# Optimization experiments

Hardware: AMD Instinct MI355X
Metric: run time of the kernel (lower is better)

Reference implementation:

```python
import jax, jax.numpy as jnp
import numpy as np

N_NODE = 50000
N_EDGE = 600000
BATCH = 64
IN_DIM = 128
OUT_DIM = 128
ATTN_DIM = 128
N_REL_IDS = 2 * 237 + 1  # 475 relation embedding rows


def setup_inputs() -> dict:
    key = jax.random.key(0)
    ks = jax.random.split(key, 16)
    s = 1.0 / np.sqrt(IN_DIM)
    return {
        "q_sub": jax.random.randint(ks[0], (BATCH,), 0, N_NODE, dtype=jnp.int32),
        "q_rel": jax.random.randint(ks[1], (BATCH,), 0, N_REL_IDS, dtype=jnp.int32),
        "r_idx": jax.random.randint(ks[2], (N_EDGE,), 0, BATCH, dtype=jnp.int32),
        "hidden": jax.random.normal(ks[3], (N_NODE, IN_DIM), dtype=jnp.float32),
        "edge_sub": jax.random.randint(ks[4], (N_EDGE,), 0, N_NODE, dtype=jnp.int32),
        "edge_rel": jax.random.randint(ks[5], (N_EDGE,), 0, N_REL_IDS, dtype=jnp.int32),
        "edge_obj": jax.random.randint(ks[6], (N_EDGE,), 0, N_NODE, dtype=jnp.int32),
        "n_node": N_NODE,
        "rela_embed": jax.random.normal(ks[7], (N_REL_IDS, IN_DIM), dtype=jnp.float32),
        "Ws": jax.random.normal(ks[8], (IN_DIM, ATTN_DIM), dtype=jnp.float32) * s,
        "Wr": jax.random.normal(ks[9], (IN_DIM, ATTN_DIM), dtype=jnp.float32) * s,
        "Wqr_w": jax.random.normal(ks[10], (IN_DIM, ATTN_DIM), dtype=jnp.float32) * s,
        "Wqr_b": jax.random.normal(ks[11], (ATTN_DIM,), dtype=jnp.float32) * s,
        "wa_w": jax.random.normal(ks[12], (ATTN_DIM,), dtype=jnp.float32) * s,
        "wa_b": jax.random.normal(ks[13], (), dtype=jnp.float32) * s,
        "Wh": jax.random.normal(ks[14], (IN_DIM, OUT_DIM), dtype=jnp.float32) * s,
    }


def reference(q_sub, q_rel, r_idx, hidden, edge_sub, edge_rel, edge_obj, n_node,
              rela_embed, Ws, Wr, Wqr_w, Wqr_b, wa_w, wa_b, Wh):
    # gather: per-edge subject hidden state and relation embedding
    hs = hidden[edge_sub]            # [E, in_dim]
    hr = rela_embed[edge_rel]        # [E, in_dim]
    h_qr = rela_embed[q_rel][r_idx]  # [E, in_dim] query-relation embed per edge
    message = hs * hr                # [E, in_dim]
    # attention MLP: sigmoid(w_alpha(relu(Ws hs + Wr hr + Wqr h_qr + b)))
    pre = jax.nn.relu(hs @ Ws + hr @ Wr + h_qr @ Wqr_w + Wqr_b)  # [E, attn]
    alpha = jax.nn.sigmoid(pre @ wa_w + wa_b)                    # [E]
    message = alpha[:, None] * message
    # scatter-add into object node buckets
    message_agg = jax.ops.segment_sum(message, edge_obj, num_segments=n_node)  # [n_node, in_dim]
    # final linear, act = identity (default)
    return message_agg @ Wh
```

## Files before the change

### kernel.cpp

```cpp
#include <hip/hip_runtime.h>

typedef float f32x4 __attribute__((ext_vector_type(4)));
typedef _Float16 f16x8 __attribute__((ext_vector_type(8)));
typedef _Float16 v2h __attribute__((ext_vector_type(2)));
typedef short s16x2 __attribute__((ext_vector_type(2)));

#define NB 128

__device__ __forceinline__ float hdot2(v2h a, v2h b, float c) {
#if __has_builtin(__builtin_amdgcn_fdot2)
  return __builtin_amdgcn_fdot2(a, b, c, false);
#else
  return c + (float)a[0] * (float)b[0] + (float)a[1] * (float)b[1];
#endif
}

__device__ __forceinline__ v2h relu2(v2h a) {
#if __has_builtin(__builtin_elementwise_max)
  const v2h z = {(_Float16)0, (_Float16)0};
  return __builtin_elementwise_max(a, z);
#else
  const v2h z = {(_Float16)0, (_Float16)0};
  s16x2 m = a > z;
  s16x2 bits = *(s16x2*)&a;
  s16x2 r = bits & m;
  return *(v2h*)&r;
#endif
}

__global__ __launch_bounds__(256) void part_hist(const int* __restrict__ eobj,
                                                 int* __restrict__ ghist,
                                                 int E, int nbkt, int chunk) {
  __shared__ int lh[128];
  const int b = blockIdx.x, t = threadIdx.x;
  for (int i = t; i < nbkt; i += 256) lh[i] = 0;
  __syncthreads();
  const int lo = b * chunk, hi = min(lo + chunk, E);
  for (int i = lo + t; i < hi; i += 256) atomicAdd(&lh[eobj[i] >> 9], 1);
  __syncthreads();
  for (int i = t; i < nbkt; i += 256) ghist[i * NB + b] = lh[i];
}

__global__ __launch_bounds__(256) void part_scatter(
    const int* __restrict__ eobj, const int* __restrict__ esub,
    const int* __restrict__ erel, const int* __restrict__ ridx,
    const int* __restrict__ qrel, const int* __restrict__ ghist,
    int* __restrict__ bstart, int* __restrict__ offs,
    int2* __restrict__ tmp, int E, int n, int nbkt, int chunk) {
  __shared__ int s[128];
  __shared__ int scur[128];
  const int b = blockIdx.x, t = threadIdx.x;

  int pre = 0, tot = 0;
  if (t < nbkt) {
#pragma unroll 8
    for (int k = 0; k < NB; ++k) {
      const int v = ghist[t * NB + k];
      pre += (k < b) ? v : 0;
      tot += v;
    }
  }
  if (t < 128) s[t] = (t < nbkt) ? tot : 0;
  __syncthreads();
  if (t < 128) {
    for (int o = 1; o < 128; o <<= 1) {
      const int a = (t >= o) ? s[t - o] : 0;
      __syncthreads();
      s[t] += a;
      __syncthreads();
    }
  } else {
    for (int o = 1; o < 128; o <<= 1) { __syncthreads(); __syncthreads(); }
  }
  if (t < nbkt) {
    const int bucket_start = s[t] - tot;
    scur[t] = bucket_start + pre;
    if (b == 0) bstart[t] = bucket_start;
  }
  if (b == 0 && t == 0) { bstart[nbkt] = E; offs[n] = E; }
  __syncthreads();

  const int lo = b * chunk, hi = min(lo + chunk, E);
  for (int i = lo + t; i < hi; i += 256) {
    const int obj = eobj[i];
    const int bkt = obj >> 9;
    const int p = atomicAdd(&scur[bkt], 1);
    tmp[p] = make_int2(esub[i], (erel[i] << 18) | (qrel[ridx[i]] << 9) | (obj & 511));
  }
}

__global__ __launch_bounds__(256) void bucket_sort(
    const int2* __restrict__ tmp, const int* __restrict__ bstart,
    int* __restrict__ offs, int2* __restrict__ ssrq, int n) {
  __shared__ int2 stage[8192];
  __shared__ int scnt[512];
  __shared__ int scur[512];
  const int b = blockIdx.x, t = threadIdx.x;
  const int s0 = bstart[b], s1 = bstart[b + 1];
  const int cnt = s1 - s0;
  const int node0 = b * 512;

  scnt[t] = 0;
  scnt[t + 256] = 0;
  __syncthreads();
  for (int i = t; i < cnt; i += 256) atomicAdd(&scnt[tmp[s0 + i].y & 511], 1);
  __syncthreads();

  const int d0 = scnt[t], d1 = scnt[t + 256];
  __syncthreads();
  for (int o = 1; o < 512; o <<= 1) {
    const int a0 = (t >= o) ? scnt[t - o] : 0;
    const int a1 = (t + 256 >= o) ? scnt[t + 256 - o] : 0;
    __syncthreads();
    scnt[t] += a0;
    scnt[t + 256] += a1;
    __syncthreads();
  }
  const int e0 = scnt[t] - d0, e1 = scnt[t + 256] - d1;
  scur[t] = e0;
  scur[t + 256] = e1;
  if (node0 + t < n) offs[node0 + t] = s0 + e0;
  if (node0 + t + 256 < n) offs[node0 + t + 256] = s0 + e1;
  __syncthreads();

  if (cnt <= 8192) {
    for (int i = t; i < cnt; i += 256) {
      const int2 p = tmp[s0 + i];
      const int q = atomicAdd(&scur[p.y & 511], 1);
      stage[q] = make_int2(p.x, p.y >> 9);
    }
    __syncthreads();
    for (int i = t; i < cnt; i += 256) ssrq[s0 + i] = stage[i];
  } else {
    for (int i = t; i < cnt; i += 256) {
      const int2 p = tmp[s0 + i];
      const int q = atomicAdd(&scur[p.y & 511], 1);
      ssrq[s0 + q] = make_int2(p.x, p.y >> 9);
    }
  }
}

__global__ __launch_bounds__(256) void prep_gemm(
    const float* __restrict__ hidden, const float* __restrict__ rela,
    const float* __restrict__ Ws, const float* __restrict__ Wr,
    const float* __restrict__ Wqr, const float* __restrict__ Wqr_b,
    _Float16* __restrict__ Hcat, _Float16* __restrict__ Rcat,
    _Float16* __restrict__ Rwqrt, int n_node, int n_rel,
    int hid_blocks, int rel_blocks) {
  __shared__ _Float16 sW[16384];
  const int bidx = blockIdx.x;
  const float* A;
  const float* W;
  const float* bias = nullptr;
  _Float16* Lo = nullptr;
  _Float16* Chi;
  int M, bb, ldc, coff;
  if (bidx < hid_blocks) {
    bb = bidx; A = hidden; W = Ws; Lo = Hcat; Chi = Hcat;
    M = n_node; ldc = 256; coff = 128;
  } else if (bidx < hid_blocks + rel_blocks) {
    bb = bidx - hid_blocks; A = rela; W = Wr; Lo = Rcat; Chi = Rcat;
    M = n_rel; ldc = 256; coff = 128;
  } else {
    bb = bidx - hid_blocks - rel_blocks; A = rela; W = Wqr; Chi = Rwqrt;
    bias = Wqr_b; M = n_rel; ldc = 128; coff = 0;
  }

  for (int i = threadIdx.x; i < 16384; i += 256) {
    const int k = i >> 7, c = i & 127;
    sW[(k >> 3) * 1024 + c * 8 + (k & 7)] = (_Float16)W[i];
  }
  __syncthreads();

  const int wv = threadIdx.x >> 6, l = threadIdx.x & 63;
  const int row = bb * 64 + wv * 16 + (l & 15);
  const int kb = (l >> 4) * 8;
  const bool rvalid = row < M;

  f16x8 a[4];
#pragma unroll
  for (int kk = 0; kk < 4; ++kk) {
    f16x8 t = {0, 0, 0, 0, 0, 0, 0, 0};
    if (rvalid) {
      const f32x4 lo = *(const f32x4*)(A + (size_t)row * 128 + kb + 32 * kk);
      const f32x4 hi = *(const f32x4*)(A + (size_t)row * 128 + kb + 32 * kk + 4);
      t[0] = (_Float16)lo[0]; t[1] = (_Float16)lo[1];
      t[2] = (_Float16)lo[2]; t[3] = (_Float16)lo[3];
      t[4] = (_Float16)hi[0]; t[5] = (_Float16)hi[1];
      t[6] = (_Float16)hi[2]; t[7] = (_Float16)hi[3];
      if (Lo) *(f16x8*)(Lo + (size_t)row * 256 + kb + 32 * kk) = t;
    }
    a[kk] = t;
  }

  f32x4 acc[8];
#pragma unroll
  for (int n = 0; n < 8; ++n) acc[n] = (f32x4){0.f, 0.f, 0.f, 0.f};
#pragma unroll
  for (int n = 0; n < 8; ++n)
#pragma unroll
    for (int kk = 0; kk < 4; ++kk) {
      const int kg = 4 * kk + (l >> 4);
      const f16x8 bfrag = *(const f16x8*)(sW + kg * 1024 + (16 * n + (l & 15)) * 8);
      acc[n] = __builtin_amdgcn_mfma_f32_16x16x32_f16(a[kk], bfrag, acc[n], 0, 0, 0);
    }

  const int orow_base = bb * 64 + wv * 16 + (l >> 4) * 4;
#pragma unroll
  for (int n = 0; n < 8; ++n) {
    const int col = 16 * n + (l & 15);
    const float badd = bias ? bias[col] : 0.0f;
#pragma unroll
    for (int r4 = 0; r4 < 4; ++r4) {
      const int orow = orow_base + r4;
      if (orow < M)
        Chi[(size_t)orow * ldc + coff + col] = (_Float16)(acc[n][r4] + badd);
    }
  }
}

__global__ __launch_bounds__(256) void gemm_final(
    const _Float16* __restrict__ agg, const float* __restrict__ Wh,
    float* __restrict__ out, int M) {
  __shared__ _Float16 sW[16384];
  for (int i = threadIdx.x; i < 16384; i += 256) {
    const int k = i >> 7, c = i & 127;
    sW[(k >> 3) * 1024 + c * 8 + (k & 7)] = (_Float16)Wh[i];
  }
  __syncthreads();

  const int wv = threadIdx.x >> 6, l = threadIdx.x & 63;
  const int row = blockIdx.x * 64 + wv * 16 + (l & 15);
  const int kb = (l >> 4) * 8;
  const bool rvalid = row < M;

  f16x8 a[4];
#pragma unroll
  for (int kk = 0; kk < 4; ++kk) {
    f16x8 t = {0, 0, 0, 0, 0, 0, 0, 0};
    if (rvalid) t = *(const f16x8*)(agg + (size_t)row * 128 + kb + 32 * kk);
    a[kk] = t;
  }

  f32x4 acc[8];
#pragma unroll
  for (int n = 0; n < 8; ++n) acc[n] = (f32x4){0.f, 0.f, 0.f, 0.f};
#pragma unroll
  for (int n = 0; n < 8; ++n)
#pragma unroll
    for (int kk = 0; kk < 4; ++kk) {
      const int kg = 4 * kk + (l >> 4);
      const f16x8 bfrag = *(const f16x8*)(sW + kg * 1024 + (16 * n + (l & 15)) * 8);
      acc[n] = __builtin_amdgcn_mfma_f32_16x16x32_f16(a[kk], bfrag, acc[n], 0, 0, 0);
    }

  const int orow_base = blockIdx.x * 64 + wv * 16 + (l >> 4) * 4;
#pragma unroll
  for (int n = 0; n < 8; ++n) {
    const int col = 16 * n + (l & 15);
#pragma unroll
    for (int r4 = 0; r4 < 4; ++r4) {
      const int orow = orow_base + r4;
      if (orow < M) out[(size_t)orow * 128 + col] = acc[n][r4];
    }
  }
}

__global__ __launch_bounds__(256) void reduce_f16(
    const int2* __restrict__ ssrq, const int* __restrict__ offs,
    const _Float16* __restrict__ Hcat, const _Float16* __restrict__ Rcat,
    const _Float16* __restrict__ Rwqrt, const float* __restrict__ wa_w,
    const float* __restrict__ wa_b_p, _Float16* __restrict__ agg, int n_node) {
  const int node = (blockIdx.x * blockDim.x + threadIdx.x) >> 6;
  if (node >= n_node) return;
  const int l = threadIdx.x & 63;
  const int g = l >> 4;
  const int d0 = (l & 15) * 8;

  v2h wa2[4];
  {
    const float4 w0 = *(const float4*)(wa_w + d0);
    const float4 w1 = *(const float4*)(wa_w + d0 + 4);
    wa2[0] = (v2h){(_Float16)w0.x, (_Float16)w0.y};
    wa2[1] = (v2h){(_Float16)w0.z, (_Float16)w0.w};
    wa2[2] = (v2h){(_Float16)w1.x, (_Float16)w1.y};
    wa2[3] = (v2h){(_Float16)w1.z, (_Float16)w1.w};
  }
  const float wab = wa_b_p[0];

  const int start = offs[node], end = offs[node + 1];
  v2h acc2[4] = {};

  for (int base = start; base < end; base += 64) {
    const int cnt = min(end - base, 64);
    int s_all = 0, rq_all = 0;
    if (l < cnt) { const int2 sr = ssrq[base + l]; s_all = sr.x; rq_all = sr.y; }
    for (int c = 0; c < cnt; c += 4) {
      const int src = c + g;
      const bool valid = src < cnt;
      const int sv = __shfl(s_all, src);
      const int rqv = __shfl(rq_all, src);
      const int rv = rqv >> 9, qv = rqv & 511;

      f32x4 rw = *(const f32x4*)(Hcat + ((size_t)sv << 8) + 128 + d0);
      f32x4 rr = *(const f32x4*)(Rcat + ((size_t)rv << 8) + 128 + d0);
      f32x4 rq = *(const f32x4*)(Rwqrt + ((size_t)qv << 7) + d0);
      f32x4 rh = *(const f32x4*)(Hcat + ((size_t)sv << 8) + d0);
      f32x4 rg = *(const f32x4*)(Rcat + ((size_t)rv << 8) + d0);
      const v2h* hw = (const v2h*)&rw;
      const v2h* hr_ = (const v2h*)&rr;
      const v2h* hq = (const v2h*)&rq;
      const v2h* hh = (const v2h*)&rh;
      const v2h* hg = (const v2h*)&rg;

      float part = 0.0f;
      v2h prod[4];
#pragma unroll
      for (int i = 0; i < 4; ++i) {
        const v2h pre = relu2(hw[i] + hr_[i] + hq[i]);
        part = hdot2(pre, wa2[i], part);
        prod[i] = hh[i] * hg[i];
      }
      part += __shfl_xor(part, 1);
      part += __shfl_xor(part, 2);
      part += __shfl_xor(part, 4);
      part += __shfl_xor(part, 8);
      const float alpha = valid ? 1.0f / (1.0f + __expf(-(part + wab))) : 0.0f;
      const _Float16 ah = (_Float16)alpha;
      const v2h alpha2 = {ah, ah};
#pragma unroll
      for (int i = 0; i < 4; ++i) acc2[i] += alpha2 * prod[i];
    }
  }

#pragma unroll
  for (int i = 0; i < 4; ++i) {
    unsigned x = *(unsigned*)&acc2[i];
    unsigned y = (unsigned)__shfl_xor((int)x, 16);
    acc2[i] += *(v2h*)&y;
    x = *(unsigned*)&acc2[i];
    y = (unsigned)__shfl_xor((int)x, 32);
    acc2[i] += *(v2h*)&y;
  }
  if (l < 16)
    *(f32x4*)(agg + (size_t)node * 128 + d0) = *(f32x4*)acc2;
}

extern "C" void kernel_launch(void* const* d_in, const int* in_sizes, int n_in,
                              void* d_out, int out_size, void* d_ws, size_t ws_size,
                              hipStream_t stream) {
  const int* q_rel = (const int*)d_in[1];
  const int* r_idx = (const int*)d_in[2];
  const float* hidden = (const float*)d_in[3];
  const int* edge_sub = (const int*)d_in[4];
  const int* edge_rel = (const int*)d_in[5];
  const int* edge_obj = (const int*)d_in[6];
  const float* rela = (const float*)d_in[8];
  const float* Ws = (const float*)d_in[9];
  const float* Wr = (const float*)d_in[10];
  const float* Wqr_w = (const float*)d_in[11];
  const float* Wqr_b = (const float*)d_in[12];
  const float* wa_w = (const float*)d_in[13];
  const float* wa_b = (const float*)d_in[14];
  const float* Wh = (const float*)d_in[15];

  const int E = in_sizes[2];
  const int n_node = in_sizes[3] / 128;
  const int n_rel = in_sizes[8] / 128;
  float* out = (float*)d_out;

  const int nbkt = (n_node + 511) / 512;
  const int chunk = (E + NB - 1) / NB;

  auto al = [](size_t x) { return (x + 511) & ~(size_t)511; };
  char* ws = (char*)d_ws;
  size_t o = 0;
  _Float16* Hcat = (_Float16*)(ws + o);  o += al((size_t)n_node * 256 * 2);
  _Float16* agg  = (_Float16*)(ws + o);  o += al((size_t)n_node * 128 * 2);
  _Float16* Rcat = (_Float16*)(ws + o);  o += al((size_t)n_rel * 256 * 2);
  _Float16* Rwqrt = (_Float16*)(ws + o); o += al((size_t)n_rel * 128 * 2);
  int* offs = (int*)(ws + o);      o += al((size_t)(n_node + 1) * 4);
  int* ghist = (int*)(ws + o);     o += al((size_t)nbkt * NB * 4);
  int* bstart = (int*)(ws + o);    o += al((size_t)(nbkt + 1) * 4);
  int2* tmp = (int2*)(ws + o);     o += al((size_t)E * 8);
  int2* ssrq = (int2*)(ws + o);    o += al((size_t)E * 8);

  part_hist<<<dim3(NB), dim3(256), 0, stream>>>(edge_obj, ghist, E, nbkt, chunk);
  part_scatter<<<dim3(NB), dim3(256), 0, stream>>>(
      edge_obj, edge_sub, edge_rel, r_idx, q_rel, ghist, bstart, offs,
      tmp, E, n_node, nbkt, chunk);
  bucket_sort<<<dim3(nbkt), dim3(256), 0, stream>>>(tmp, bstart, offs, ssrq, n_node);

  const int hid_blocks = (n_node + 63) / 64;
  const int rel_blocks = (n_rel + 63) / 64;
  prep_gemm<<<dim3(hid_blocks + 2 * rel_blocks), dim3(256), 0, stream>>>(
      hidden, rela, Ws, Wr, Wqr_w, Wqr_b, Hcat, Rcat, Rwqrt,
      n_node, n_rel, hid_blocks, rel_blocks);

  const int rblocks = (n_node * 64 + 255) / 256;
  reduce_f16<<<dim3(rblocks), dim3(256), 0, stream>>>(
      ssrq, offs, Hcat, Rcat, Rwqrt, wa_w, wa_b, agg, n_node);

  gemm_final<<<dim3(hid_blocks), dim3(256), 0, stream>>>(agg, Wh, out, n_node);
}
```

Before: 227.9 us.

## Compute edge attention in edge order and pack alpha with relation into sort keys

Per-edge attention is moved out of the segmented reduction into a new kernel that runs in original edge order. That kernel is fused with the partition histogram and writes an f16 alpha packed with the relation id per edge. The sort now carries the edge index, and bucket_sort looks up the packed alpha/relation word. The reduction then only gathers the H and R rows and does a multiply-accumulate. Hcat and Rcat are split into separate 128-wide arrays. This trades an extra pass over E edges and more gathers of the projected rows for a lighter, less irregular per-node reduction, at the cost of additional kernels and an extra global alpha array.

```diff
diff --git a/kernel.cpp b/kernel.cpp
--- a/kernel.cpp
+++ b/kernel.cpp
@@ -6,6 +6,8 @@
 typedef short s16x2 __attribute__((ext_vector_type(2)));
 
 #define NB 128
+
+union h16bits { _Float16 h; unsigned short u; };
 
 __device__ __forceinline__ float hdot2(v2h a, v2h b, float c) {
 #if __has_builtin(__builtin_amdgcn_fdot2)
@@ -28,124 +30,13 @@
 #endif
 }
 
-__global__ __launch_bounds__(256) void part_hist(const int* __restrict__ eobj,
-                                                 int* __restrict__ ghist,
-                                                 int E, int nbkt, int chunk) {
-  __shared__ int lh[128];
-  const int b = blockIdx.x, t = threadIdx.x;
-  for (int i = t; i < nbkt; i += 256) lh[i] = 0;
-  __syncthreads();
-  const int lo = b * chunk, hi = min(lo + chunk, E);
-  for (int i = lo + t; i < hi; i += 256) atomicAdd(&lh[eobj[i] >> 9], 1);
-  __syncthreads();
-  for (int i = t; i < nbkt; i += 256) ghist[i * NB + b] = lh[i];
-}
-
-__global__ __launch_bounds__(256) void part_scatter(
-    const int* __restrict__ eobj, const int* __restrict__ esub,
-    const int* __restrict__ erel, const int* __restrict__ ridx,
-    const int* __restrict__ qrel, const int* __restrict__ ghist,
-    int* __restrict__ bstart, int* __restrict__ offs,
-    int2* __restrict__ tmp, int E, int n, int nbkt, int chunk) {
-  __shared__ int s[128];
-  __shared__ int scur[128];
-  const int b = blockIdx.x, t = threadIdx.x;
-
-  int pre = 0, tot = 0;
-  if (t < nbkt) {
-#pragma unroll 8
-    for (int k = 0; k < NB; ++k) {
-      const int v = ghist[t * NB + k];
-      pre += (k < b) ? v : 0;
-      tot += v;
-    }
-  }
-  if (t < 128) s[t] = (t < nbkt) ? tot : 0;
-  __syncthreads();
-  if (t < 128) {
-    for (int o = 1; o < 128; o <<= 1) {
-      const int a = (t >= o) ? s[t - o] : 0;
-      __syncthreads();
-      s[t] += a;
-      __syncthreads();
-    }
-  } else {
-    for (int o = 1; o < 128; o <<= 1) { __syncthreads(); __syncthreads(); }
-  }
-  if (t < nbkt) {
-    const int bucket_start = s[t] - tot;
-    scur[t] = bucket_start + pre;
-    if (b == 0) bstart[t] = bucket_start;
-  }
-  if (b == 0 && t == 0) { bstart[nbkt] = E; offs[n] = E; }
-  __syncthreads();
-
-  const int lo = b * chunk, hi = min(lo + chunk, E);
-  for (int i = lo + t; i < hi; i += 256) {
-    const int obj = eobj[i];
-    const int bkt = obj >> 9;
-    const int p = atomicAdd(&scur[bkt], 1);
-    tmp[p] = make_int2(esub[i], (erel[i] << 18) | (qrel[ridx[i]] << 9) | (obj & 511));
-  }
-}
-
-__global__ __launch_bounds__(256) void bucket_sort(
-    const int2* __restrict__ tmp, const int* __restrict__ bstart,
-    int* __restrict__ offs, int2* __restrict__ ssrq, int n) {
-  __shared__ int2 stage[8192];
-  __shared__ int scnt[512];
-  __shared__ int scur[512];
-  const int b = blockIdx.x, t = threadIdx.x;
-  const int s0 = bstart[b], s1 = bstart[b + 1];
-  const int cnt = s1 - s0;
-  const int node0 = b * 512;
-
-  scnt[t] = 0;
-  scnt[t + 256] = 0;
-  __syncthreads();
-  for (int i = t; i < cnt; i += 256) atomicAdd(&scnt[tmp[s0 + i].y & 511], 1);
-  __syncthreads();
-
-  const int d0 = scnt[t], d1 = scnt[t + 256];
-  __syncthreads();
-  for (int o = 1; o < 512; o <<= 1) {
-    const int a0 = (t >= o) ? scnt[t - o] : 0;
-    const int a1 = (t + 256 >= o) ? scnt[t + 256 - o] : 0;
-    __syncthreads();
-    scnt[t] += a0;
-    scnt[t + 256] += a1;
-    __syncthreads();
-  }
-  const int e0 = scnt[t] - d0, e1 = scnt[t + 256] - d1;
-  scur[t] = e0;
-  scur[t + 256] = e1;
-  if (node0 + t < n) offs[node0 + t] = s0 + e0;
-  if (node0 + t + 256 < n) offs[node0 + t + 256] = s0 + e1;
-  __syncthreads();
-
-  if (cnt <= 8192) {
-    for (int i = t; i < cnt; i += 256) {
-      const int2 p = tmp[s0 + i];
-      const int q = atomicAdd(&scur[p.y & 511], 1);
-      stage[q] = make_int2(p.x, p.y >> 9);
-    }
-    __syncthreads();
-    for (int i = t; i < cnt; i += 256) ssrq[s0 + i] = stage[i];
-  } else {
-    for (int i = t; i < cnt; i += 256) {
-      const int2 p = tmp[s0 + i];
-      const int q = atomicAdd(&scur[p.y & 511], 1);
-      ssrq[s0 + q] = make_int2(p.x, p.y >> 9);
-    }
-  }
-}
-
 __global__ __launch_bounds__(256) void prep_gemm(
     const float* __restrict__ hidden, const float* __restrict__ rela,
     const float* __restrict__ Ws, const float* __restrict__ Wr,
     const float* __restrict__ Wqr, const float* __restrict__ Wqr_b,
-    _Float16* __restrict__ Hcat, _Float16* __restrict__ Rcat,
-    _Float16* __restrict__ Rwqrt, int n_node, int n_rel,
+    _Float16* __restrict__ Hlo, _Float16* __restrict__ Hws,
+    _Float16* __restrict__ Rlo, _Float16* __restrict__ Rwr,
+    _Float16* __restrict__ Rwqr, int n_node, int n_rel,
     int hid_blocks, int rel_blocks) {
   __shared__ _Float16 sW[16384];
   const int bidx = blockIdx.x;
@@ -153,17 +44,15 @@
   const float* W;
   const float* bias = nullptr;
   _Float16* Lo = nullptr;
-  _Float16* Chi;
-  int M, bb, ldc, coff;
+  _Float16* C;
+  int M, bb;
   if (bidx < hid_blocks) {
-    bb = bidx; A = hidden; W = Ws; Lo = Hcat; Chi = Hcat;
-    M = n_node; ldc = 256; coff = 128;
+    bb = bidx; A = hidden; W = Ws; Lo = Hlo; C = Hws; M = n_node;
   } else if (bidx < hid_blocks + rel_blocks) {
-    bb = bidx - hid_blocks; A = rela; W = Wr; Lo = Rcat; Chi = Rcat;
-    M = n_rel; ldc = 256; coff = 128;
+    bb = bidx - hid_blocks; A = rela; W = Wr; Lo = Rlo; C = Rwr; M = n_rel;
   } else {
-    bb = bidx - hid_blocks - rel_blocks; A = rela; W = Wqr; Chi = Rwqrt;
-    bias = Wqr_b; M = n_rel; ldc = 128; coff = 0;
+    bb = bidx - hid_blocks - rel_blocks; A = rela; W = Wqr; C = Rwqr;
+    bias = Wqr_b; M = n_rel;
   }
 
   for (int i = threadIdx.x; i < 16384; i += 256) {
@@ -188,7 +77,7 @@
       t[2] = (_Float16)lo[2]; t[3] = (_Float16)lo[3];
       t[4] = (_Float16)hi[0]; t[5] = (_Float16)hi[1];
       t[6] = (_Float16)hi[2]; t[7] = (_Float16)hi[3];
-      if (Lo) *(f16x8*)(Lo + (size_t)row * 256 + kb + 32 * kk) = t;
+      if (Lo) *(f16x8*)(Lo + (size_t)row * 128 + kb + 32 * kk) = t;
     }
     a[kk] = t;
   }
@@ -214,68 +103,37 @@
     for (int r4 = 0; r4 < 4; ++r4) {
       const int orow = orow_base + r4;
       if (orow < M)
-        Chi[(size_t)orow * ldc + coff + col] = (_Float16)(acc[n][r4] + badd);
-    }
-  }
-}
-
-__global__ __launch_bounds__(256) void gemm_final(
-    const _Float16* __restrict__ agg, const float* __restrict__ Wh,
-    float* __restrict__ out, int M) {
-  __shared__ _Float16 sW[16384];
-  for (int i = threadIdx.x; i < 16384; i += 256) {
-    const int k = i >> 7, c = i & 127;
-    sW[(k >> 3) * 1024 + c * 8 + (k & 7)] = (_Float16)Wh[i];
-  }
-  __syncthreads();
-
-  const int wv = threadIdx.x >> 6, l = threadIdx.x & 63;
-  const int row = blockIdx.x * 64 + wv * 16 + (l & 15);
-  const int kb = (l >> 4) * 8;
-  const bool rvalid = row < M;
-
-  f16x8 a[4];
-#pragma unroll
-  for (int kk = 0; kk < 4; ++kk) {
-    f16x8 t = {0, 0, 0, 0, 0, 0, 0, 0};
-    if (rvalid) t = *(const f16x8*)(agg + (size_t)row * 128 + kb + 32 * kk);
-    a[kk] = t;
-  }
-
-  f32x4 acc[8];
-#pragma unroll
-  for (int n = 0; n < 8; ++n) acc[n] = (f32x4){0.f, 0.f, 0.f, 0.f};
-#pragma unroll
-  for (int n = 0; n < 8; ++n)
-#pragma unroll
-    for (int kk = 0; kk < 4; ++kk) {
-      const int kg = 4 * kk + (l >> 4);
-      const f16x8 bfrag = *(const f16x8*)(sW + kg * 1024 + (16 * n + (l & 15)) * 8);
-      acc[n] = __builtin_amdgcn_mfma_f32_16x16x32_f16(a[kk], bfrag, acc[n], 0, 0, 0);
-    }
-
-  const int orow_base = blockIdx.x * 64 + wv * 16 + (l >> 4) * 4;
-#pragma unroll
-  for (int n = 0; n < 8; ++n) {
-    const int col = 16 * n + (l & 15);
-#pragma unroll
-    for (int r4 = 0; r4 < 4; ++r4) {
-      const int orow = orow_base + r4;
-      if (orow < M) out[(size_t)orow * 128 + col] = acc[n][r4];
-    }
-  }
-}
-
-__global__ __launch_bounds__(256) void reduce_f16(
-    const int2* __restrict__ ssrq, const int* __restrict__ offs,
-    const _Float16* __restrict__ Hcat, const _Float16* __restrict__ Rcat,
-    const _Float16* __restrict__ Rwqrt, const float* __restrict__ wa_w,
-    const float* __restrict__ wa_b_p, _Float16* __restrict__ agg, int n_node) {
-  const int node = (blockIdx.x * blockDim.x + threadIdx.x) >> 6;
-  if (node >= n_node) return;
-  const int l = threadIdx.x & 63;
+        C[(size_t)orow * 128 + col] = (_Float16)(acc[n][r4] + badd);
+    }
+  }
+}
+
+__global__ __launch_bounds__(256) void hist_alpha(
+    const int* __restrict__ eobj, const int* __restrict__ esub,
+    const int* __restrict__ erel, const int* __restrict__ ridx,
+    const int* __restrict__ qrel, const _Float16* __restrict__ Hws,
+    const _Float16* __restrict__ Rwr, const _Float16* __restrict__ Rwqr,
+    const float* __restrict__ wa_w, const float* __restrict__ wa_b_p,
+    int* __restrict__ ghist, int* __restrict__ ar,
+    int E, int nbkt, int chunk) {
+  __shared__ int lh[128];
+  const int bidx = blockIdx.x, t = threadIdx.x;
+
+  if (bidx < NB) {
+    for (int i = t; i < nbkt; i += 256) lh[i] = 0;
+    __syncthreads();
+    const int lo = bidx * chunk, hi = min(lo + chunk, E);
+    for (int i = lo + t; i < hi; i += 256) atomicAdd(&lh[eobj[i] >> 9], 1);
+    __syncthreads();
+    for (int i = t; i < nbkt; i += 256) ghist[i * NB + bidx] = lh[i];
+    return;
+  }
+
+  const int wv = t >> 6, l = t & 63;
   const int g = l >> 4;
   const int d0 = (l & 15) * 8;
+  const int aw = (bidx - NB) * 4 + wv;
+  const int nwaves = (gridDim.x - NB) * 4;
 
   v2h wa2[4];
   {
@@ -288,48 +146,182 @@
   }
   const float wab = wa_b_p[0];
 
+  for (int base = aw * 64; base < E; base += nwaves * 64) {
+    const int cnt = min(E - base, 64);
+    int s = 0, r = 0, q = 0;
+    if (l < cnt) {
+      const int i = base + l;
+      s = esub[i];
+      r = erel[i];
+      q = qrel[ridx[i]];
+    }
+    for (int c = 0; c < cnt; c += 4) {
+      const int src = c + g;
+      const bool valid = src < cnt;
+      const int sv = __shfl(s, src);
+      const int rv = __shfl(r, src);
+      const int qv = __shfl(q, src);
+
+      const f32x4 rw = *(const f32x4*)(Hws + ((size_t)sv << 7) + d0);
+      const f32x4 rr = *(const f32x4*)(Rwr + ((size_t)rv << 7) + d0);
+      const f32x4 rq = *(const f32x4*)(Rwqr + ((size_t)qv << 7) + d0);
+      const v2h* hw = (const v2h*)&rw;
+      const v2h* hr_ = (const v2h*)&rr;
+      const v2h* hq = (const v2h*)&rq;
+
+      float part = 0.0f;
+#pragma unroll
+      for (int i = 0; i < 4; ++i)
+        part = hdot2(relu2(hw[i] + hr_[i] + hq[i]), wa2[i], part);
+      part += __shfl_xor(part, 1);
+      part += __shfl_xor(part, 2);
+      part += __shfl_xor(part, 4);
+      part += __shfl_xor(part, 8);
+
+      if (valid && (l & 15) == 0) {
+        const float alpha = 1.0f / (1.0f + __expf(-(part + wab)));
+        h16bits hb;
+        hb.h = (_Float16)alpha;
+        ar[base + src] = (rv << 16) | hb.u;
+      }
+    }
+  }
+}
+
+__global__ __launch_bounds__(256) void part_scatter(
+    const int* __restrict__ eobj, const int* __restrict__ esub,
+    const int* __restrict__ ghist, int* __restrict__ bstart,
+    int* __restrict__ offs, int2* __restrict__ tmp,
+    int E, int n, int nbkt, int chunk) {
+  __shared__ int s[128];
+  __shared__ int scur[128];
+  const int b = blockIdx.x, t = threadIdx.x;
+
+  int pre = 0, tot = 0;
+  if (t < nbkt) {
+#pragma unroll 8
+    for (int k = 0; k < NB; ++k) {
+      const int v = ghist[t * NB + k];
+      pre += (k < b) ? v : 0;
+      tot += v;
+    }
+  }
+  if (t < 128) s[t] = (t < nbkt) ? tot : 0;
+  __syncthreads();
+  if (t < 128) {
+    for (int o = 1; o < 128; o <<= 1) {
+      const int a = (t >= o) ? s[t - o] : 0;
+      __syncthreads();
+      s[t] += a;
+      __syncthreads();
+    }
+  } else {
+    for (int o = 1; o < 128; o <<= 1) { __syncthreads(); __syncthreads(); }
+  }
+  if (t < nbkt) {
+    const int bucket_start = s[t] - tot;
+    scur[t] = bucket_start + pre;
+    if (b == 0) bstart[t] = bucket_start;
+  }
+  if (b == 0 && t == 0) { bstart[nbkt] = E; offs[n] = E; }
+  __syncthreads();
+
+  const int lo = b * chunk, hi = min(lo + chunk, E);
+  for (int i = lo + t; i < hi; i += 256) {
+    const int obj = eobj[i];
+    const int bkt = obj >> 9;
+    const int p = atomicAdd(&scur[bkt], 1);
+    tmp[p] = make_int2(esub[i], (i << 9) | (obj & 511));
+  }
+}
+
+__global__ __launch_bounds__(256) void bucket_sort(
+    const int2* __restrict__ tmp, const int* __restrict__ ar,
+    const int* __restrict__ bstart, int* __restrict__ offs,
+    int2* __restrict__ ssrq, int n) {
+  __shared__ int2 stage[8192];
+  __shared__ int scnt[512];
+  __shared__ int scur[512];
+  const int b = blockIdx.x, t = threadIdx.x;
+  const int s0 = bstart[b], s1 = bstart[b + 1];
+  const int cnt = s1 - s0;
+  const int node0 = b * 512;
+
+  scnt[t] = 0;
+  scnt[t + 256] = 0;
+  __syncthreads();
+  for (int i = t; i < cnt; i += 256) atomicAdd(&scnt[tmp[s0 + i].y & 511], 1);
+  __syncthreads();
+
+  const int d0 = scnt[t], d1 = scnt[t + 256];
+  __syncthreads();
+  for (int o = 1; o < 512; o <<= 1) {
+    const int a0 = (t >= o) ? scnt[t - o] : 0;
+    const int a1 = (t + 256 >= o) ? scnt[t + 256 - o] : 0;
+    __syncthreads();
+    scnt[t] += a0;
+    scnt[t + 256] += a1;
+    __syncthreads();
+  }
+  const int e0 = scnt[t] - d0, e1 = scnt[t + 256] - d1;
+  scur[t] = e0;
+  scur[t + 256] = e1;
+  if (node0 + t < n) offs[node0 + t] = s0 + e0;
+  if (node0 + t + 256 < n) offs[node0 + t + 256] = s0 + e1;
+  __syncthreads();
+
+  if (cnt <= 8192) {
+    for (int i = t; i < cnt; i += 256) {
+      const int2 p = tmp[s0 + i];
+      const int q = atomicAdd(&scur[p.y & 511], 1);
+      stage[q] = make_int2(p.x, ar[p.y >> 9]);
+    }
+    __syncthreads();
+    for (int i = t; i < cnt; i += 256) ssrq[s0 + i] = stage[i];
+  } else {
+    for (int i = t; i < cnt; i += 256) {
+      const int2 p = tmp[s0 + i];
+      const int q = atomicAdd(&scur[p.y & 511], 1);
+      ssrq[s0 + q] = make_int2(p.x, ar[p.y >> 9]);
+    }
+  }
+}
+
+__global__ __launch_bounds__(256) void reduce_lite(
+    const int2* __restrict__ ssrq, const int* __restrict__ offs,
+    const _Float16* __restrict__ Hlo, const _Float16* __restrict__ Rlo,
+    _Float16* __restrict__ agg, int n_node) {
+  const int node = (blockIdx.x * blockDim.x + threadIdx.x) >> 6;
+  if (node >= n_node) return;
+  const int l = threadIdx.x & 63;
+  const int g = l >> 4;
+  const int d0 = (l & 15) * 8;
+
   const int start = offs[node], end = offs[node + 1];
   v2h acc2[4] = {};
 
   for (int base = start; base < end; base += 64) {
     const int cnt = min(end - base, 64);
-    int s_all = 0, rq_all = 0;
-    if (l < cnt) { const int2 sr = ssrq[base + l]; s_all = sr.x; rq_all = sr.y; }
+    int s_all = 0, ra_all = 0;
+    if (l < cnt) { const int2 sr = ssrq[base + l]; s_all = sr.x; ra_all = sr.y; }
     for (int c = 0; c < cnt; c += 4) {
       const int src = c + g;
       const bool valid = src < cnt;
       const int sv = __shfl(s_all, src);
-      const int rqv = __shfl(rq_all, src);
-      const int rv = rqv >> 9, qv = rqv & 511;
-
-      f32x4 rw = *(const f32x4*)(Hcat + ((size_t)sv << 8) + 128 + d0);
-      f32x4 rr = *(const f32x4*)(Rcat + ((size_t)rv << 8) + 128 + d0);
-      f32x4 rq = *(const f32x4*)(Rwqrt + ((size_t)qv << 7) + d0);
-      f32x4 rh = *(const f32x4*)(Hcat + ((size_t)sv << 8) + d0);
-      f32x4 rg = *(const f32x4*)(Rcat + ((size_t)rv << 8) + d0);
-      const v2h* hw = (const v2h*)&rw;
-      const v2h* hr_ = (const v2h*)&rr;
-      const v2h* hq = (const v2h*)&rq;
+      const int rav = __shfl(ra_all, src);
+      const int rv = rav >> 16;
+
+      h16bits hb;
+      hb.u = (unsigned short)(rav & 0xffff);
+      const _Float16 ah = valid ? hb.h : (_Float16)0;
+      const v2h alpha2 = {ah, ah};
+
+      const f32x4 rh = *(const f32x4*)(Hlo + ((size_t)sv << 7) + d0);
+      const f32x4 rg = *(const f32x4*)(Rlo + ((size_t)rv << 7) + d0);
       const v2h* hh = (const v2h*)&rh;
       const v2h* hg = (const v2h*)&rg;
-
-      float part = 0.0f;
-      v2h prod[4];
-#pragma unroll
-      for (int i = 0; i < 4; ++i) {
-        const v2h pre = relu2(hw[i] + hr_[i] + hq[i]);
-        part = hdot2(pre, wa2[i], part);
-        prod[i] = hh[i] * hg[i];
-      }
-      part += __shfl_xor(part, 1);
-      part += __shfl_xor(part, 2);
-      part += __shfl_xor(part, 4);
-      part += __shfl_xor(part, 8);
-      const float alpha = valid ? 1.0f / (1.0f + __expf(-(part + wab))) : 0.0f;
-      const _Float16 ah = (_Float16)alpha;
-      const v2h alpha2 = {ah, ah};
-#pragma unroll
-      for (int i = 0; i < 4; ++i) acc2[i] += alpha2 * prod[i];
+#pragma unroll
+      for (int i = 0; i < 4; ++i) acc2[i] += alpha2 * (hh[i] * hg[i]);
     }
   }
 
@@ -344,6 +336,53 @@
   }
   if (l < 16)
     *(f32x4*)(agg + (size_t)node * 128 + d0) = *(f32x4*)acc2;
+}
+
+__global__ __launch_bounds__(256) void gemm_final(
+    const _Float16* __restrict__ agg, const float* __restrict__ Wh,
+    float* __restrict__ out, int M) {
+  __shared__ _Float16 sW[16384];
+  for (int i = threadIdx.x; i < 16384; i += 256) {
+    const int k = i >> 7, c = i & 127;
+    sW[(k >> 3) * 1024 + c * 8 + (k & 7)] = (_Float16)Wh[i];
+  }
+  __syncthreads();
+
+  const int wv = threadIdx.x >> 6, l = threadIdx.x & 63;
+  const int row = blockIdx.x * 64 + wv * 16 + (l & 15);
+  const int kb = (l >> 4) * 8;
+  const bool rvalid = row < M;
+
+  f16x8 a[4];
+#pragma unroll
+  for (int kk = 0; kk < 4; ++kk) {
+    f16x8 t = {0, 0, 0, 0, 0, 0, 0, 0};
+    if (rvalid) t = *(const f16x8*)(agg + (size_t)row * 128 + kb + 32 * kk);
+    a[kk] = t;
+  }
+
+  f32x4 acc[8];
+#pragma unroll
+  for (int n = 0; n < 8; ++n) acc[n] = (f32x4){0.f, 0.f, 0.f, 0.f};
+#pragma unroll
+  for (int n = 0; n < 8; ++n)
+#pragma unroll
+    for (int kk = 0; kk < 4; ++kk) {
+      const int kg = 4 * kk + (l >> 4);
+      const f16x8 bfrag = *(const f16x8*)(sW + kg * 1024 + (16 * n + (l & 15)) * 8);
+      acc[n] = __builtin_amdgcn_mfma_f32_16x16x32_f16(a[kk], bfrag, acc[n], 0, 0, 0);
+    }
+
+  const int orow_base = blockIdx.x * 64 + wv * 16 + (l >> 4) * 4;
+#pragma unroll
+  for (int n = 0; n < 8; ++n) {
+    const int col = 16 * n + (l & 15);
+#pragma unroll
+    for (int r4 = 0; r4 < 4; ++r4) {
+      const int orow = orow_base + r4;
+      if (orow < M) out[(size_t)orow * 128 + col] = acc[n][r4];
+    }
+  }
 }
 
 extern "C" void kernel_launch(void* const* d_in, const int* in_sizes, int n_in,
@@ -375,31 +414,39 @@
   auto al = [](size_t x) { return (x + 511) & ~(size_t)511; };
   char* ws = (char*)d_ws;
   size_t o = 0;
-  _Float16* Hcat = (_Float16*)(ws + o);  o += al((size_t)n_node * 256 * 2);
-  _Float16* agg  = (_Float16*)(ws + o);  o += al((size_t)n_node * 128 * 2);
-  _Float16* Rcat = (_Float16*)(ws + o);  o += al((size_t)n_rel * 256 * 2);
-  _Float16* Rwqrt = (_Float16*)(ws + o); o += al((size_t)n_rel * 128 * 2);
+  _Float16* Hlo = (_Float16*)(ws + o);   o += al((size_t)n_node * 128 * 2);
+  _Float16* Hws = (_Float16*)(ws + o);   o += al((size_t)n_node * 128 * 2);
+  _Float16* agg = (_Float16*)(ws + o);   o += al((size_t)n_node * 128 * 2);
+  _Float16* Rlo = (_Float16*)(ws + o);   o += al((size_t)n_rel * 128 * 2);
+  _Float16* Rwr = (_Float16*)(ws + o);   o += al((size_t)n_rel * 128 * 2);
+  _Float16* Rwqr = (_Float16*)(ws + o);  o += al((size_t)n_rel * 128 * 2);
   int* offs = (int*)(ws + o);      o += al((size_t)(n_node + 1) * 4);
   int* ghist = (int*)(ws + o);     o += al((size_t)nbkt * NB * 4);
   int* bstart = (int*)(ws + o);    o += al((size_t)(nbkt + 1) * 4);
+  int* ar = (int*)(ws + o);        o += al((size_t)E * 4);
   int2* tmp = (int2*)(ws + o);     o += al((size_t)E * 8);
   int2* ssrq = (int2*)(ws + o);    o += al((size_t)E * 8);
 
-  part_hist<<<dim3(NB), dim3(256), 0, stream>>>(edge_obj, ghist, E, nbkt, chunk);
-  part_scatter<<<dim3(NB), dim3(256), 0, stream>>>(
-      edge_obj, edge_sub, edge_rel, r_idx, q_rel, ghist, bstart, offs,
-      tmp, E, n_node, nbkt, chunk);
-  bucket_sort<<<dim3(nbkt), dim3(256), 0, stream>>>(tmp, bstart, offs, ssrq, n_node);
-
   const int hid_blocks = (n_node + 63) / 64;
   const int rel_blocks = (n_rel + 63) / 64;
+
   prep_gemm<<<dim3(hid_blocks + 2 * rel_blocks), dim3(256), 0, stream>>>(
-      hidden, rela, Ws, Wr, Wqr_w, Wqr_b, Hcat, Rcat, Rwqrt,
+      hidden, rela, Ws, Wr, Wqr_w, Wqr_b, Hlo, Hws, Rlo, Rwr, Rwqr,
       n_node, n_rel, hid_blocks, rel_blocks);
 
+  hist_alpha<<<dim3(NB + 2048), dim3(256), 0, stream>>>(
+      edge_obj, edge_sub, edge_rel, r_idx, q_rel, Hws, Rwr, Rwqr,
+      wa_w, wa_b, ghist, ar, E, nbkt, chunk);
+
+  part_scatter<<<dim3(NB), dim3(256), 0, stream>>>(
+      edge_obj, edge_sub, ghist, bstart, offs, tmp, E, n_node, nbkt, chunk);
+
+  bucket_sort<<<dim3(nbkt), dim3(256), 0, stream>>>(tmp, ar, bstart, offs,
+                                                    ssrq, n_node);
+
   const int rblocks = (n_node * 64 + 255) / 256;
-  reduce_f16<<<dim3(rblocks), dim3(256), 0, stream>>>(
-      ssrq, offs, Hcat, Rcat, Rwqrt, wa_w, wa_b, agg, n_node);
+  reduce_lite<<<dim3(rblocks), dim3(256), 0, stream>>>(
+      ssrq, offs, Hlo, Rlo, agg, n_node);
 
   gemm_final<<<dim3(hid_blocks), dim3(256), 0, stream>>>(agg, Wh, out, n_node);
 }
```

Measured after the change: 231.8 us. Within noise of the previous version (+1.7%).
